# Kernel tuning notes

Measured on AMD Instinct MI355X. Metric: run time of the kernel, lower is better.

Reference implementation:

```python
import jax, jax.numpy as jnp
import numpy as np

N, E, D_IN, D_OUT = 50000, 800000, 32, 64


def setup_inputs() -> dict:
    key = jax.random.key(0)
    k1, k2, k3 = jax.random.split(key, 3)
    x = jax.random.normal(k1, (N, D_IN), dtype=jnp.float32)
    edge_index = jax.random.randint(k2, (2, E), 0, N)
    W = jax.random.normal(k3, (D_IN, D_OUT), dtype=jnp.float32) / np.sqrt(D_IN).astype(np.float32)
    b = jnp.zeros((D_OUT,), dtype=jnp.float32)
    return {"x": x, "edge_index": edge_index, "W": W, "b": b}


def gcn_conv(x, edge_index, W, b):
    n = x.shape[0]
    loop = jnp.arange(n)
    src = jnp.concatenate([edge_index[0], loop])  # message sources (x_j)
    dst = jnp.concatenate([edge_index[1], loop])  # aggregation targets
    xw = x @ W  # [N, D_OUT]
    deg = jax.ops.segment_sum(jnp.ones(src.shape[0], dtype=xw.dtype), dst, num_segments=n)
    dinv = jnp.where(deg > 0, jax.lax.rsqrt(jnp.where(deg > 0, deg, 1.0)), 0.0)
    norm = dinv[src] * dinv[dst]  # [E+N]
    msg = xw[src] * norm[:, None]  # gather + scale
    out = jax.ops.segment_sum(msg, dst, num_segments=n)  # scatter-add aggregate
    return out + b


def reference(x, edge_index, W, b):
    h = jax.nn.relu(gcn_conv(x, edge_index, W, b))
    # InnerProductDecoder over given edges: sigmoid(<h_i, h_j>)
    logits = jnp.sum(h[edge_index[0]] * h[edge_index[1]], axis=-1)  # [E]
    adj_pred = jax.nn.sigmoid(logits) + 1e-15
    return (adj_pred, edge_index)
```

## Files before the change

kernel.cpp:

```cpp
#include <hip/hip_runtime.h>
#include <hip/hip_fp8.h>

#define D_IN 32
#define D_OUT 64
#define NBMAX 800
#define BIN_BLKS 128
#define COPY_BLKS 784
#define CAP 32
#define BCAP 1280

__device__ __forceinline__ unsigned char f2fp8(float f) {
    __hip_fp8_e4m3 v(f);
    return (unsigned char)v.__x;
}
__device__ __forceinline__ float fp82f(unsigned char u) {
    __hip_fp8_e4m3 v;
    v.__x = (__hip_fp8_storage_t)u;
    return (float)v;
}
__device__ __forceinline__ float dot4fp8(unsigned int ua, unsigned int ub) {
    float s = 0.f;
#pragma unroll
    for (int k = 0; k < 4; ++k) {
        __hip_fp8_e4m3 fa, fb;
        fa.__x = (__hip_fp8_storage_t)(unsigned char)(ua >> (8 * k));
        fb.__x = (__hip_fp8_storage_t)(unsigned char)(ub >> (8 * k));
        s += (float)fa * (float)fb;
    }
    return s;
}

__global__ void __launch_bounds__(256) k_bin(const int* __restrict__ src,
                                             const int* __restrict__ dst,
                                             int* __restrict__ cellcnt,
                                             int* __restrict__ cells,
                                             const int* __restrict__ ei,
                                             float* __restrict__ outE,
                                             int E, int NB, int chunk) {
    int t = threadIdx.x;
    if (blockIdx.x >= BIN_BLKS) {
        int ct = (blockIdx.x - BIN_BLKS) * 256 + t;
        int cstride = COPY_BLKS * 256;
        int n4 = (2 * E) >> 2;
        const int4* ei4 = (const int4*)ei;
        float4* o4 = (float4*)outE;
        for (int i = ct; i < n4; i += cstride) {
            int4 v = ei4[i];
            o4[i] = make_float4((float)v.x, (float)v.y, (float)v.z, (float)v.w);
        }
        for (int i = n4 * 4 + ct; i < 2 * E; i += cstride) outE[i] = (float)ei[i];
        return;
    }
    __shared__ int cur[NBMAX];
    int blk = blockIdx.x;
    int s0 = blk * chunk;
    int s1 = s0 + chunk; if (s1 > E) s1 = E;
    for (int i = t; i < NB; i += 256) cur[i] = 0;
    __syncthreads();
    if (s0 < E) {
        for (int k = s0 + t * 8; k < s1; k += 2048) {
            if (k + 7 < s1) {
                int4 sa = *(const int4*)(src + k);
                int4 sb = *(const int4*)(src + k + 4);
                int4 da = *(const int4*)(dst + k);
                int4 db = *(const int4*)(dst + k + 4);
                int s8[8] = {sa.x, sa.y, sa.z, sa.w, sb.x, sb.y, sb.z, sb.w};
                int d8[8] = {da.x, da.y, da.z, da.w, db.x, db.y, db.z, db.w};
#pragma unroll
                for (int u = 0; u < 8; ++u) {
                    int d = d8[u], bin = d >> 6;
                    int pos = atomicAdd(&cur[bin], 1);
                    if (pos < CAP)
                        cells[((size_t)bin * BIN_BLKS + blk) * CAP + pos] = (s8[u] << 6) | (d & 63);
                }
            } else {
                for (int e = k; e < s1; ++e) {
                    int d = dst[e], bin = d >> 6;
                    int pos = atomicAdd(&cur[bin], 1);
                    if (pos < CAP)
                        cells[((size_t)bin * BIN_BLKS + blk) * CAP + pos] = (src[e] << 6) | (d & 63);
                }
            }
        }
    }
    __syncthreads();
    for (int i = t; i < NB; i += 256) cellcnt[(size_t)blk * NB + i] = min(cur[i], CAP);
}

__global__ void __launch_bounds__(256) k_build(const float* __restrict__ x,
                                               const float* __restrict__ W,
                                               const int* __restrict__ cellcnt,
                                               const int* __restrict__ cells,
                                               float* __restrict__ dinv,
                                               int* __restrict__ offs, int* __restrict__ ends,
                                               int* __restrict__ srcs,
                                               unsigned char* __restrict__ xws, int N, int NB) {
    __shared__ float Ws[D_IN * D_OUT];
    __shared__ float xs[64 * D_IN];
    __shared__ int ebuf[BIN_BLKS * CAP];
    __shared__ int ccnt[BIN_BLKS], coff[BIN_BLKS + 1];
    __shared__ int lcnt[64], lofs[65], lcur[64];
    __shared__ float ds[64];
    int bin = blockIdx.x, t = threadIdx.x;
    int node0 = bin * 64;
    for (int i = t; i < D_IN * D_OUT; i += 256) Ws[i] = W[i];
    for (int i = t; i < 64 * (D_IN / 4); i += 256) {
        int r = i >> 3, q = i & 7;
        int node = node0 + r;
        float4 v = make_float4(0.f, 0.f, 0.f, 0.f);
        if (node < N) v = *(const float4*)(x + (size_t)node * D_IN + q * 4);
        *(float4*)(xs + r * D_IN + q * 4) = v;
    }
    if (t < 64) { lcnt[t] = 0; lcur[t] = 0; }
    if (t < BIN_BLKS) ccnt[t] = cellcnt[(size_t)t * NB + bin];
    __syncthreads();
    if (t == 0) {
        int r = 0;
#pragma unroll
        for (int i = 0; i < BIN_BLKS; ++i) { coff[i] = r; r += ccnt[i]; }
        coff[BIN_BLKS] = r;
    }
    __syncthreads();
    const int* crow = cells + (size_t)bin * BIN_BLKS * CAP;
#pragma unroll
    for (int i = 0; i < (BIN_BLKS * CAP) / 256; ++i) {
        int idx = i * 256 + t;
        int cell = idx >> 5, pos = idx & (CAP - 1);
        if (pos < ccnt[cell]) {
            int p = crow[idx];
            ebuf[coff[cell] + pos] = p;
            atomicAdd(&lcnt[p & 63], 1);
        }
    }
    __syncthreads();
    int ns = coff[BIN_BLKS];
    if (t == 0) {
        int r = 0;
#pragma unroll
        for (int i = 0; i < 64; ++i) { lofs[i] = r; r += lcnt[i]; }
        lofs[64] = r;
    }
    __syncthreads();
    int binbase = bin * BCAP;
    if (t < 64) {
        float d = rsqrtf((float)(lcnt[t] + 1));
        ds[t] = d;
        int node = node0 + t;
        if (node < N) {
            dinv[node] = d;
            offs[node] = binbase + lofs[t];
            ends[node] = binbase + lofs[t + 1];
        }
    }
    __syncthreads();
    for (int k = t; k < ns; k += 256) {
        int p = ebuf[k];
        int d = p & 63;
        int slot = atomicAdd(&lcur[d], 1);
        srcs[binbase + lofs[d] + slot] = p >> 6;
    }
#pragma unroll
    for (int i = 0; i < 16; ++i) {
        int idx = i * 256 + t;
        int ln = idx >> 6, c = idx & 63;
        int node = node0 + ln;
        if (node < N) {
            float s = 0.f;
#pragma unroll
            for (int k = 0; k < D_IN; ++k) s += xs[ln * D_IN + k] * Ws[k * D_OUT + c];
            xws[(size_t)node * D_OUT + c] = f2fp8(s * ds[ln]);
        }
    }
}

__global__ void k_agg(const unsigned char* __restrict__ xws, const float* __restrict__ dinv,
                      const int* __restrict__ offs, const int* __restrict__ ends,
                      const int* __restrict__ srcs,
                      const float* __restrict__ b, unsigned char* __restrict__ h, int n) {
    int g = blockIdx.x * blockDim.x + threadIdx.x;
    int d = g >> 6, c = g & 63;
    if (d >= n) return;
    float dd = dinv[d];
    float a0 = fp82f(xws[(size_t)d * D_OUT + c]);
    float a1 = 0.f, a2 = 0.f, a3 = 0.f;
    int kend = ends[d];
    for (int k = offs[d]; k < kend; k += 8) {
        int s[8];
        float v[8];
#pragma unroll
        for (int u = 0; u < 8; ++u) {
            int t = k + u;
            s[u] = srcs[t < kend ? t : kend - 1];
        }
#pragma unroll
        for (int u = 0; u < 8; ++u) {
            float xv = fp82f(xws[(size_t)s[u] * D_OUT + c]);
            v[u] = (k + u < kend) ? xv : 0.f;
        }
        a0 += v[0]; a1 += v[1]; a2 += v[2]; a3 += v[3];
        a0 += v[4]; a1 += v[5]; a2 += v[6]; a3 += v[7];
    }
    float r = dd * ((a0 + a1) + (a2 + a3)) + b[c];
    h[(size_t)d * D_OUT + c] = f2fp8(r > 0.f ? r : 0.f);
}

__global__ void k_decode(const int* __restrict__ e0, const int* __restrict__ e1,
                         const unsigned char* __restrict__ h, float* __restrict__ out,
                         int E, int halfE) {
    int g = blockIdx.x * blockDim.x + threadIdx.x;
    int pair = g >> 1, q = g & 1;
    if (pair >= halfE) return;
    int ea = pair;
    int eb = pair + halfE;
    bool hasB = eb < E;
    int ia = e0[ea], ja = e1[ea];
    int ib = hasB ? e0[eb] : ia;
    int jb = hasB ? e1[eb] : ja;
    const uint4* hia = (const uint4*)(h + (size_t)ia * D_OUT + q * 32);
    const uint4* hja = (const uint4*)(h + (size_t)ja * D_OUT + q * 32);
    const uint4* hib = (const uint4*)(h + (size_t)ib * D_OUT + q * 32);
    const uint4* hjb = (const uint4*)(h + (size_t)jb * D_OUT + q * 32);
    uint4 a0 = hia[0], a1 = hia[1];
    uint4 b0 = hja[0], b1 = hja[1];
    uint4 c0 = hib[0], c1 = hib[1];
    uint4 d0 = hjb[0], d1 = hjb[1];
    float pa = dot4fp8(a0.x, b0.x) + dot4fp8(a0.y, b0.y)
             + dot4fp8(a0.z, b0.z) + dot4fp8(a0.w, b0.w)
             + dot4fp8(a1.x, b1.x) + dot4fp8(a1.y, b1.y)
             + dot4fp8(a1.z, b1.z) + dot4fp8(a1.w, b1.w);
    float pb = dot4fp8(c0.x, d0.x) + dot4fp8(c0.y, d0.y)
             + dot4fp8(c0.z, d0.z) + dot4fp8(c0.w, d0.w)
             + dot4fp8(c1.x, d1.x) + dot4fp8(c1.y, d1.y)
             + dot4fp8(c1.z, d1.z) + dot4fp8(c1.w, d1.w);
    pa += __shfl_xor(pa, 1, 64);
    pb += __shfl_xor(pb, 1, 64);
    if (q == 0) {
        out[ea] = 1.0f / (1.0f + expf(-pa)) + 1e-15f;
        if (hasB) out[eb] = 1.0f / (1.0f + expf(-pb)) + 1e-15f;
    }
}

extern "C" void kernel_launch(void* const* d_in, const int* in_sizes, int n_in,
                              void* d_out, int out_size, void* d_ws, size_t ws_size,
                              hipStream_t stream) {
    const float* x = (const float*)d_in[0];
    const int*   ei = (const int*)d_in[1];
    const float* W = (const float*)d_in[2];
    const float* b = (const float*)d_in[3];

    const int N = in_sizes[0] / D_IN;
    const int E = in_sizes[1] / 2;
    const size_t NF = (size_t)N * D_OUT;
    const int NB = (N + 63) >> 6;

    float* out = (float*)d_out;

    char* base = (char*)d_ws;
    unsigned char* xws     = (unsigned char*)base;
    unsigned char* h       = (unsigned char*)(base + NF);
    float*         dinv    = (float*)(base + NF * 2);
    int*           offs    = (int*)(base + NF * 2 + (size_t)N * 4);
    int*           ends    = offs + N;
    int*           cellcnt = ends + N;
    int*           srcs    = cellcnt + (size_t)BIN_BLKS * NB;
    int*           cells   = srcs + (size_t)NB * BCAP;

    const int* srcv = ei;
    const int* dstv = ei + E;

    const int B = 256;
    const int gNF = (int)((NF + B - 1) / B);
    const int halfE = (E + 1) / 2;
    const int gD  = (int)(((long long)halfE * 2 + B - 1) / B);
    const int chunk = ((E + BIN_BLKS - 1) / BIN_BLKS + 7) & ~7;

    k_bin   <<<BIN_BLKS + COPY_BLKS, B, 0, stream>>>(srcv, dstv, cellcnt, cells,
                                                     ei, out + E, E, NB, chunk);
    k_build <<<NB,  B, 0, stream>>>(x, W, cellcnt, cells, dinv, offs, ends, srcs, xws, N, NB);
    k_agg   <<<gNF, B, 0, stream>>>(xws, dinv, offs, ends, srcs, b, h, N);
    k_decode<<<gD,  B, 0, stream>>>(srcv, dstv, h, out, E, halfE);
}
```

Before: 79.55 us.

## Move dense x@W into idle copy blocks of binning kernel, store bf16

Computes the dense x@W product in the copy blocks of the binning kernel and writes an intermediate bf16 buffer. The build kernel then only reads it back, scales by dinv and quantizes to fp8. The goal is to overlap the GEMM with the latency-bound binning pass and shorten the build kernel's critical path. In exchange it adds an extra bf16 write and read of N*64 values, plus an extra rounding step before fp8. It also relies on COPY_BLKS*64 covering N: 784*64 = 50176, which is at least 50000.

```diff
diff --git a/kernel.cpp b/kernel.cpp
--- a/kernel.cpp
+++ b/kernel.cpp
@@ -18,6 +18,14 @@
     v.__x = (__hip_fp8_storage_t)u;
     return (float)v;
 }
+__device__ __forceinline__ float bf2f(unsigned short u) {
+    return __uint_as_float(((unsigned int)u) << 16);
+}
+__device__ __forceinline__ unsigned short f2bf(float f) {
+    unsigned int x = __float_as_uint(f);
+    x += 0x7fff + ((x >> 16) & 1);
+    return (unsigned short)(x >> 16);
+}
 __device__ __forceinline__ float dot4fp8(unsigned int ua, unsigned int ub) {
     float s = 0.f;
 #pragma unroll
@@ -36,10 +44,38 @@
                                              int* __restrict__ cells,
                                              const int* __restrict__ ei,
                                              float* __restrict__ outE,
-                                             int E, int NB, int chunk) {
+                                             const float* __restrict__ x,
+                                             const float* __restrict__ W,
+                                             unsigned short* __restrict__ xwb,
+                                             int N, int E, int NB, int chunk) {
     int t = threadIdx.x;
     if (blockIdx.x >= BIN_BLKS) {
-        int ct = (blockIdx.x - BIN_BLKS) * 256 + t;
+        int cb = blockIdx.x - BIN_BLKS;
+        __shared__ float Ws[D_IN * D_OUT];
+        __shared__ float xs[64 * D_IN];
+        int node0 = cb * 64;
+        for (int i = t; i < D_IN * D_OUT; i += 256) Ws[i] = W[i];
+        for (int i = t; i < 64 * (D_IN / 4); i += 256) {
+            int r = i >> 3, q = i & 7;
+            int node = node0 + r;
+            float4 v = make_float4(0.f, 0.f, 0.f, 0.f);
+            if (node < N) v = *(const float4*)(x + (size_t)node * D_IN + q * 4);
+            *(float4*)(xs + r * D_IN + q * 4) = v;
+        }
+        __syncthreads();
+#pragma unroll
+        for (int i = 0; i < 16; ++i) {
+            int idx = i * 256 + t;
+            int ln = idx >> 6, c = idx & 63;
+            int node = node0 + ln;
+            if (node < N) {
+                float s = 0.f;
+#pragma unroll
+                for (int k = 0; k < D_IN; ++k) s += xs[ln * D_IN + k] * Ws[k * D_OUT + c];
+                xwb[(size_t)node * D_OUT + c] = f2bf(s);
+            }
+        }
+        int ct = cb * 256 + t;
         int cstride = COPY_BLKS * 256;
         int n4 = (2 * E) >> 2;
         const int4* ei4 = (const int4*)ei;
@@ -87,30 +123,19 @@
     for (int i = t; i < NB; i += 256) cellcnt[(size_t)blk * NB + i] = min(cur[i], CAP);
 }
 
-__global__ void __launch_bounds__(256) k_build(const float* __restrict__ x,
-                                               const float* __restrict__ W,
+__global__ void __launch_bounds__(256) k_build(const unsigned short* __restrict__ xwb,
                                                const int* __restrict__ cellcnt,
                                                const int* __restrict__ cells,
                                                float* __restrict__ dinv,
                                                int* __restrict__ offs, int* __restrict__ ends,
                                                int* __restrict__ srcs,
                                                unsigned char* __restrict__ xws, int N, int NB) {
-    __shared__ float Ws[D_IN * D_OUT];
-    __shared__ float xs[64 * D_IN];
     __shared__ int ebuf[BIN_BLKS * CAP];
     __shared__ int ccnt[BIN_BLKS], coff[BIN_BLKS + 1];
     __shared__ int lcnt[64], lofs[65], lcur[64];
     __shared__ float ds[64];
     int bin = blockIdx.x, t = threadIdx.x;
     int node0 = bin * 64;
-    for (int i = t; i < D_IN * D_OUT; i += 256) Ws[i] = W[i];
-    for (int i = t; i < 64 * (D_IN / 4); i += 256) {
-        int r = i >> 3, q = i & 7;
-        int node = node0 + r;
-        float4 v = make_float4(0.f, 0.f, 0.f, 0.f);
-        if (node < N) v = *(const float4*)(x + (size_t)node * D_IN + q * 4);
-        *(float4*)(xs + r * D_IN + q * 4) = v;
-    }
     if (t < 64) { lcnt[t] = 0; lcur[t] = 0; }
     if (t < BIN_BLKS) ccnt[t] = cellcnt[(size_t)t * NB + bin];
     __syncthreads();
@@ -164,12 +189,8 @@
         int idx = i * 256 + t;
         int ln = idx >> 6, c = idx & 63;
         int node = node0 + ln;
-        if (node < N) {
-            float s = 0.f;
-#pragma unroll
-            for (int k = 0; k < D_IN; ++k) s += xs[ln * D_IN + k] * Ws[k * D_OUT + c];
-            xws[(size_t)node * D_OUT + c] = f2fp8(s * ds[ln]);
-        }
+        if (node < N)
+            xws[(size_t)node * D_OUT + c] = f2fp8(bf2f(xwb[(size_t)node * D_OUT + c]) * ds[ln]);
     }
 }
 
@@ -256,14 +277,15 @@
     float* out = (float*)d_out;
 
     char* base = (char*)d_ws;
-    unsigned char* xws     = (unsigned char*)base;
-    unsigned char* h       = (unsigned char*)(base + NF);
-    float*         dinv    = (float*)(base + NF * 2);
-    int*           offs    = (int*)(base + NF * 2 + (size_t)N * 4);
-    int*           ends    = offs + N;
-    int*           cellcnt = ends + N;
-    int*           srcs    = cellcnt + (size_t)BIN_BLKS * NB;
-    int*           cells   = srcs + (size_t)NB * BCAP;
+    unsigned char*  xws     = (unsigned char*)base;
+    unsigned char*  h       = (unsigned char*)(base + NF);
+    unsigned short* xwb     = (unsigned short*)(base + NF * 2);
+    float*          dinv    = (float*)(base + NF * 4);
+    int*            offs    = (int*)(base + NF * 4 + (size_t)N * 4);
+    int*            ends    = offs + N;
+    int*            cellcnt = ends + N;
+    int*            srcs    = cellcnt + (size_t)BIN_BLKS * NB;
+    int*            cells   = srcs + (size_t)NB * BCAP;
 
     const int* srcv = ei;
     const int* dstv = ei + E;
@@ -275,8 +297,8 @@
     const int chunk = ((E + BIN_BLKS - 1) / BIN_BLKS + 7) & ~7;
 
     k_bin   <<<BIN_BLKS + COPY_BLKS, B, 0, stream>>>(srcv, dstv, cellcnt, cells,
-                                                     ei, out + E, E, NB, chunk);
-    k_build <<<NB,  B, 0, stream>>>(x, W, cellcnt, cells, dinv, offs, ends, srcs, xws, N, NB);
+                                                     ei, out + E, x, W, xwb, N, E, NB, chunk);
+    k_build <<<NB,  B, 0, stream>>>(xwb, cellcnt, cells, dinv, offs, ends, srcs, xws, N, NB);
     k_agg   <<<gNF, B, 0, stream>>>(xws, dinv, offs, ends, srcs, b, h, N);
     k_decode<<<gD,  B, 0, stream>>>(srcv, dstv, h, out, E, halfE);
 }
```

New measurement: 78.62 us. About the same (-1.2%).
